# Kernel tuning notes

Measured on AMD Instinct MI355X. Metric: run time of the kernel, lower is better.

Reference implementation:

```python
import jax, jax.numpy as jnp
import numpy as np

H = 16  # heads
K_POLY = 3  # K from init


def setup_inputs() -> dict:
    key = jax.random.key(0)
    ks = jax.random.split(key, 6)
    B, N, D = 4, 1024, 1024
    s = 1.0 / np.sqrt(D)
    return {
        "x": jax.random.normal(ks[0], (B, N, D), jnp.float32),
        "Wq": jax.random.normal(ks[1], (D, D), jnp.float32) * s,
        "bq": jnp.zeros((D,), jnp.float32),
        "Wk": jax.random.normal(ks[2], (D, D), jnp.float32) * s,
        "bk": jnp.zeros((D,), jnp.float32),
        "Wv": jax.random.normal(ks[3], (D, D), jnp.float32) * s,
        "bv": jnp.zeros((D,), jnp.float32),
        "Wo": jax.random.normal(ks[4], (D, D), jnp.float32) * s,
        "bo": jnp.zeros((D,), jnp.float32),
        "w0": jnp.zeros((H,), jnp.float32),
        "w1": jnp.ones((H,), jnp.float32),
        "wK": jnp.zeros((H,), jnp.float32),
    }


def reference(x, Wq, bq, Wk, bk, Wv, bv, Wo, bo, w0, w1, wK):
    B, N, D = x.shape
    d = D // H
    # projections -> [B, H, N, d]
    def proj(W, b):
        return (x @ W + b).reshape(B, N, H, d).transpose(0, 2, 1, 3)
    q = proj(Wq, bq)
    k = proj(Wk, bk)
    v = proj(Wv, bv)
    att = jax.nn.softmax(jnp.einsum('bhnd,bhmd->bhnm', q, k) / jnp.sqrt(jnp.float32(d)), axis=-1)
    att2 = jnp.einsum('bhnm,bhmk->bhnk', att, att)  # att @ att
    attK = att + (K_POLY - 1) * (att2 - att)
    eye = jnp.eye(N, dtype=x.dtype)  # [N, N]
    gf = (w0[None, :, None, None] * eye[None, None]
          + w1[None, :, None, None] * att
          + wK[None, :, None, None] * attK)
    out = jnp.einsum('bhnm,bhmd->bhnd', gf, v)  # [B, H, N, d]
    out = out.transpose(0, 2, 1, 3).reshape(B, N, D)
    return out @ Wo + bo
```

## Files before the change

### kernel.cpp

```cpp
#include <hip/hip_runtime.h>

typedef unsigned short u16;
typedef unsigned int u32;
typedef __attribute__((ext_vector_type(8))) short short8;
typedef __attribute__((ext_vector_type(4))) float f32x4;

__device__ __forceinline__ u16 f2bf(float f) {
  union { float f; u32 u; } c; c.f = f;
  u32 u = c.u;
  u += 0x7fffu + ((u >> 16) & 1u);
  return (u16)(u >> 16);
}
__device__ __forceinline__ float bf2f(u16 h) {
  union { u32 u; float f; } c; c.u = ((u32)h) << 16;
  return c.f;
}

#define GLDS16(g, l)                                                          \
  __builtin_amdgcn_global_load_lds(                                           \
      (const __attribute__((address_space(1))) u32*)(g),                      \
      (__attribute__((address_space(3))) u32*)(l), 16, 0, 0)

#define EXP_SCALE 0.18033688011112042f

__global__ __launch_bounds__(256) void k_cast_x(const float* __restrict__ x,
                                                u16* __restrict__ xb) {
  int i = blockIdx.x * 256 + threadIdx.x;
  float4 v = ((const float4*)x)[i];
  short4 s;
  s.x = (short)f2bf(v.x); s.y = (short)f2bf(v.y);
  s.z = (short)f2bf(v.z); s.w = (short)f2bf(v.w);
  *(short4*)(xb + (size_t)i * 4) = s;
}

__global__ __launch_bounds__(256) void k_trans_w(
    const float* __restrict__ W0, const float* __restrict__ W1,
    const float* __restrict__ W2, const float* __restrict__ W3,
    u16* __restrict__ T0, u16* __restrict__ T1, u16* __restrict__ T2,
    u16* __restrict__ T3) {
  const float* W = blockIdx.z == 0 ? W0 : blockIdx.z == 1 ? W1 : blockIdx.z == 2 ? W2 : W3;
  u16* T = blockIdx.z == 0 ? T0 : blockIdx.z == 1 ? T1 : blockIdx.z == 2 ? T2 : T3;
  __shared__ float tile[32][33];
  int r0 = blockIdx.y * 32, c0 = blockIdx.x * 32;
  int tid = threadIdx.x;
  for (int i = tid; i < 1024; i += 256) {
    int r = i >> 5, c = i & 31;
    tile[r][c] = W[(size_t)(r0 + r) * 1024 + c0 + c];
  }
  __syncthreads();
  for (int i = tid; i < 1024; i += 256) {
    int r = i >> 5, c = i & 31;
    T[(size_t)(c0 + r) * 1024 + r0 + c] = f2bf(tile[c][r]);
  }
}

__device__ __forceinline__ void core128x128_p3(const u16* __restrict__ A,
                                               const u16* __restrict__ Bt, int K,
                                               f32x4 (&acc)[4][4], u16* As,
                                               u16* Bs) {
  const int tid = threadIdx.x;
  const int lane = tid & 63;
  const int wm = tid >> 7, wn = (tid >> 6) & 1;
  const int fr = lane & 15, fg = lane >> 4;
  const int sr = tid >> 2, sc = (tid & 3) * 8;
#pragma unroll
  for (int i = 0; i < 4; ++i)
#pragma unroll
    for (int j = 0; j < 4; ++j) acc[i][j] = f32x4{0.f, 0.f, 0.f, 0.f};

  auto stage = [&](int t, int slot) {
    u16* as = As + slot * 4096;
    u16* bs = Bs + slot * 4096;
    const int k0 = t * 32 + sc;
    GLDS16(A + (size_t)sr * K + k0, as + tid * 8);
    GLDS16(A + (size_t)(sr + 64) * K + k0, as + (256 + tid) * 8);
    GLDS16(Bt + (size_t)sr * K + k0, bs + tid * 8);
    GLDS16(Bt + (size_t)(sr + 64) * K + k0, bs + (256 + tid) * 8);
  };
  auto compute = [&](int slot) {
    const u16* as = As + slot * 4096;
    const u16* bs = Bs + slot * 4096;
    short8 af[4], bfv[4];
#pragma unroll
    for (int i = 0; i < 4; ++i)
      af[i] = *(const short8*)(as + (wm * 64 + i * 16 + fr) * 32 + fg * 8);
#pragma unroll
    for (int j = 0; j < 4; ++j)
      bfv[j] = *(const short8*)(bs + (wn * 64 + j * 16 + fr) * 32 + fg * 8);
#pragma unroll
    for (int i = 0; i < 4; ++i)
#pragma unroll
      for (int j = 0; j < 4; ++j)
        acc[i][j] = __builtin_amdgcn_mfma_f32_16x16x32_bf16(af[i], bfv[j],
                                                            acc[i][j], 0, 0, 0);
  };

  const int NS = K / 32;
  stage(0, 0);
  stage(1, 1);
  int cs = 0, ss = 2;
  for (int t = 0; t + 2 < NS; ++t) {
    asm volatile("s_waitcnt vmcnt(4) lgkmcnt(0)" ::: "memory");
    __builtin_amdgcn_s_barrier();
    asm volatile("" ::: "memory");
    stage(t + 2, ss);
    compute(cs);
    cs = cs == 2 ? 0 : cs + 1;
    ss = ss == 2 ? 0 : ss + 1;
  }
  asm volatile("s_waitcnt vmcnt(4) lgkmcnt(0)" ::: "memory");
  __builtin_amdgcn_s_barrier();
  asm volatile("" ::: "memory");
  compute(cs);
  cs = cs == 2 ? 0 : cs + 1;
  asm volatile("s_waitcnt vmcnt(0) lgkmcnt(0)" ::: "memory");
  __builtin_amdgcn_s_barrier();
  asm volatile("" ::: "memory");
  compute(cs);
}

__device__ __forceinline__ void core128x64_p3(const u16* __restrict__ A,
                                              const u16* __restrict__ Bt, int K,
                                              f32x4 (&acc)[2][4], u16* As,
                                              u16* Bs) {
  const int tid = threadIdx.x;
  const int lane = tid & 63;
  const int w = tid >> 6;
  const int fr = lane & 15, fg = lane >> 4;
  const int sr = tid >> 2, sc = (tid & 3) * 8;
#pragma unroll
  for (int i = 0; i < 2; ++i)
#pragma unroll
    for (int j = 0; j < 4; ++j) acc[i][j] = f32x4{0.f, 0.f, 0.f, 0.f};

  auto stage = [&](int t, int slot) {
    u16* as = As + slot * 4096;
    u16* bs = Bs + slot * 2048;
    const int k0 = t * 32 + sc;
    GLDS16(A + (size_t)sr * K + k0, as + tid * 8);
    GLDS16(A + (size_t)(sr + 64) * K + k0, as + (256 + tid) * 8);
    GLDS16(Bt + (size_t)sr * K + k0, bs + tid * 8);
  };
  auto compute = [&](int slot) {
    const u16* as = As + slot * 4096;
    const u16* bs = Bs + slot * 2048;
    short8 af[2], bfv[4];
#pragma unroll
    for (int i = 0; i < 2; ++i)
      af[i] = *(const short8*)(as + (w * 32 + i * 16 + fr) * 32 + fg * 8);
#pragma unroll
    for (int j = 0; j < 4; ++j)
      bfv[j] = *(const short8*)(bs + (j * 16 + fr) * 32 + fg * 8);
#pragma unroll
    for (int i = 0; i < 2; ++i)
#pragma unroll
      for (int j = 0; j < 4; ++j)
        acc[i][j] = __builtin_amdgcn_mfma_f32_16x16x32_bf16(af[i], bfv[j],
                                                            acc[i][j], 0, 0, 0);
  };

  const int NS = K / 32;
  stage(0, 0);
  stage(1, 1);
  int cs = 0, ss = 2;
  for (int t = 0; t + 2 < NS; ++t) {
    asm volatile("s_waitcnt vmcnt(3) lgkmcnt(0)" ::: "memory");
    __builtin_amdgcn_s_barrier();
    asm volatile("" ::: "memory");
    stage(t + 2, ss);
    compute(cs);
    cs = cs == 2 ? 0 : cs + 1;
    ss = ss == 2 ? 0 : ss + 1;
  }
  asm volatile("s_waitcnt vmcnt(3) lgkmcnt(0)" ::: "memory");
  __builtin_amdgcn_s_barrier();
  asm volatile("" ::: "memory");
  compute(cs);
  cs = cs == 2 ? 0 : cs + 1;
  asm volatile("s_waitcnt vmcnt(0) lgkmcnt(0)" ::: "memory");
  __builtin_amdgcn_s_barrier();
  asm volatile("" ::: "memory");
  compute(cs);
}

__global__ __launch_bounds__(256) void k_proj(
    const u16* __restrict__ xb, const u16* __restrict__ WqT,
    const u16* __restrict__ WkT, const u16* __restrict__ WvT,
    const float* __restrict__ bq, const float* __restrict__ bk,
    const float* __restrict__ bv, u16* __restrict__ qh, u16* __restrict__ kh,
    u16* __restrict__ vh, u16* __restrict__ vT) {
  __shared__ __align__(16) u16 As[3 * 128 * 32];
  __shared__ __align__(16) u16 Bs[3 * 128 * 32];
  const int li = blockIdx.x + 32 * (blockIdx.y + 8 * blockIdx.z);
  const int cx = li & 7, jb = li >> 3;
  const int m0 = (cx * 4 + (jb & 3)) * 128;
  const int n0 = ((jb >> 2) & 7) * 128;
  const int which = jb >> 5;
  const u16* Bt = which == 0 ? WqT : which == 1 ? WkT : WvT;
  const float* bias = which == 0 ? bq : which == 1 ? bk : bv;
  f32x4 acc[4][4];
  core128x128_p3(xb + (size_t)m0 * 1024, Bt + (size_t)n0 * 1024, 1024, acc, As, Bs);
  const int tid = threadIdx.x, lane = tid & 63;
  const int wm = tid >> 7, wn = (tid >> 6) & 1, fr = lane & 15, fg = lane >> 4;
#pragma unroll
  for (int i = 0; i < 4; ++i)
#pragma unroll
    for (int j2 = 0; j2 < 4; ++j2) {
      int n = n0 + wn * 64 + j2 * 16 + fr;
      float bb = bias[n];
      int h = n >> 6, dc = n & 63;
#pragma unroll
      for (int r = 0; r < 4; ++r) {
        int m = m0 + wm * 64 + i * 16 + fg * 4 + r;
        int b = m >> 10, nr = m & 1023;
        int z = b * 16 + h;
        float val = acc[i][j2][r] + bb;
        u16 bv16 = f2bf(val);
        if (which == 0) {
          qh[((size_t)z * 1024 + nr) * 64 + dc] = bv16;
        } else if (which == 1) {
          kh[((size_t)z * 1024 + nr) * 64 + dc] = bv16;
        } else {
          vh[((size_t)z * 1024 + nr) * 64 + dc] = bv16;
          vT[((size_t)z * 64 + dc) * 1024 + nr] = bv16;
        }
      }
    }
}

__global__ __launch_bounds__(256) void k_pass1(
    const u16* __restrict__ qh, const u16* __restrict__ kh,
    const u16* __restrict__ vT, u16* __restrict__ P1T,
    u16* __restrict__ P1h, float* __restrict__ mlinv) {
  __shared__ __align__(16) u16 Ks[64 * 64];
  __shared__ __align__(16) u16 Vs[64 * 64];
  __shared__ __align__(16) u16 Ps[4][16 * 64];
  const int li = blockIdx.x + 16 * blockIdx.y;
  const int cx = li & 7, jb = li >> 3;
  const int z = cx * 8 + (jb >> 4);
  const int m0 = (jb & 15) * 64;
  const int tid = threadIdx.x, lane = tid & 63, w = tid >> 6;
  const int fr = lane & 15, fg = lane >> 4;
  const int row0 = m0 + w * 16;
  const u16* qbase = qh + (size_t)z * 65536;
  const u16* kbase = kh + (size_t)z * 65536;
  const u16* vbase = vT + (size_t)z * 65536;
  u16* myP = &Ps[w][0];

  short8 qf[2];
#pragma unroll
  for (int kc = 0; kc < 2; ++kc)
    qf[kc] = *(const short8*)(qbase + (size_t)(row0 + fr) * 64 + (kc * 4 + fg) * 8);

  f32x4 o[4];
  float rs[4];
#pragma unroll
  for (int ct = 0; ct < 4; ++ct) o[ct] = f32x4{0.f, 0.f, 0.f, 0.f};
#pragma unroll
  for (int r = 0; r < 4; ++r) rs[r] = 0.f;

  for (int t = 0; t < 16; ++t) {
    const int kv0 = t * 64;
#pragma unroll
    for (int it = 0; it < 2; ++it) {
      int idx = it * 256 + tid;
      int row = idx >> 3, cc = idx & 7;
      GLDS16(kbase + (size_t)(kv0 + row) * 64 + ((cc ^ (row & 7)) * 8),
             Ks + idx * 8);
      GLDS16(vbase + (size_t)row * 1024 + kv0 + ((cc ^ (row & 7)) * 8),
             Vs + idx * 8);
    }
    __syncthreads();
#pragma unroll
    for (int ct = 0; ct < 4; ++ct) {
      int krow = ct * 16 + fr;
      short8 k0 = *(const short8*)(Ks + krow * 64 + ((fg ^ (krow & 7)) * 8));
      short8 k1 = *(const short8*)(Ks + krow * 64 + (((4 + fg) ^ (krow & 7)) * 8));
      f32x4 s = __builtin_amdgcn_mfma_f32_16x16x32_bf16(
          qf[0], k0, f32x4{0.f, 0.f, 0.f, 0.f}, 0, 0, 0);
      s = __builtin_amdgcn_mfma_f32_16x16x32_bf16(qf[1], k1, s, 0, 0, 0);
      int pcol = ct * 16 + fr;
      int cc = pcol >> 3;
#pragma unroll
      for (int r = 0; r < 4; ++r) {
        float e = __builtin_exp2f(s[r] * EXP_SCALE);
        rs[r] += e;
        int prow = fg * 4 + r;
        myP[prow * 64 + ((cc ^ (prow & 7)) * 8) + (pcol & 7)] = f2bf(e);
      }
    }
    asm volatile("s_waitcnt lgkmcnt(0)" ::: "memory");
    short8 p0 = *(const short8*)(myP + fr * 64 + ((fg ^ (fr & 7)) * 8));
    short8 p1 = *(const short8*)(myP + fr * 64 + (((4 + fg) ^ (fr & 7)) * 8));
#pragma unroll
    for (int ct = 0; ct < 4; ++ct) {
      int vrow = ct * 16 + fr;
      short8 v0 = *(const short8*)(Vs + vrow * 64 + ((fg ^ (vrow & 7)) * 8));
      short8 v1 = *(const short8*)(Vs + vrow * 64 + (((4 + fg) ^ (vrow & 7)) * 8));
      o[ct] = __builtin_amdgcn_mfma_f32_16x16x32_bf16(p0, v0, o[ct], 0, 0, 0);
      o[ct] = __builtin_amdgcn_mfma_f32_16x16x32_bf16(p1, v1, o[ct], 0, 0, 0);
    }
    __syncthreads();
  }
#pragma unroll
  for (int off = 1; off < 16; off <<= 1)
#pragma unroll
    for (int r = 0; r < 4; ++r) rs[r] += __shfl_xor(rs[r], off, 64);
  float linv[4];
#pragma unroll
  for (int r = 0; r < 4; ++r) linv[r] = 1.f / rs[r];
#pragma unroll
  for (int ct = 0; ct < 4; ++ct) {
    union { u16 u[4]; short4 s4; } pk;
#pragma unroll
    for (int r = 0; r < 4; ++r) {
      u16 b_ = f2bf(o[ct][r] * linv[r]);
      pk.u[r] = b_;
      myP[(fg * 4 + r) * 64 + ct * 16 + fr] = b_;
    }
    *(short4*)(P1T + ((size_t)z * 64 + ct * 16 + fr) * 1024 + row0 + fg * 4) =
        pk.s4;
  }
  asm volatile("s_waitcnt lgkmcnt(0)" ::: "memory");
  {
    int r_ = lane >> 2;
#pragma unroll
    for (int ch2 = 0; ch2 < 2; ++ch2) {
      int ch = (lane & 3) * 2 + ch2;
      int4 vv = *(const int4*)(myP + r_ * 64 + ch * 8);
      *(int4*)(P1h + ((size_t)z * 1024 + row0 + r_) * 64 + ch * 8) = vv;
    }
  }
  if (fr == 0) {
#pragma unroll
    for (int r = 0; r < 4; ++r)
      mlinv[(size_t)z * 1024 + row0 + fg * 4 + r] = linv[r];
  }
}

__global__ __launch_bounds__(256) void k_pass2(
    const u16* __restrict__ qh, const u16* __restrict__ kh,
    const u16* __restrict__ P1T, const u16* __restrict__ vh,
    const u16* __restrict__ P1h, const float* __restrict__ mlinv,
    const float* __restrict__ w0, const float* __restrict__ w1,
    const float* __restrict__ wK, u16* __restrict__ OH) {
  __shared__ __align__(16) u16 Ks[64 * 64];
  __shared__ __align__(16) u16 Ts[64 * 64];
  __shared__ __align__(16) u16 Ps[4][16 * 64];
  const int li = blockIdx.x + 16 * blockIdx.y;
  const int cx = li & 7, jb = li >> 3;
  const int z = cx * 8 + (jb >> 4);
  const int m0 = (jb & 15) * 64;
  const int tid = threadIdx.x, lane = tid & 63, w = tid >> 6;
  const int fr = lane & 15, fg = lane >> 4;
  const int row0 = m0 + w * 16;
  const int h = z & 15, b = z >> 4;
  const float cw0 = w0[h], cw1 = w1[h] - wK[h], cw2 = 2.f * wK[h];
  const u16* qbase = qh + (size_t)z * 65536;
  const u16* kbase = kh + (size_t)z * 65536;
  const u16* tbase = P1T + (size_t)z * 65536;
  u16* myP = &Ps[w][0];

  short8 qf[2];
#pragma unroll
  for (int kc = 0; kc < 2; ++kc)
    qf[kc] = *(const short8*)(qbase + (size_t)(row0 + fr) * 64 + (kc * 4 + fg) * 8);
  float lrow[4];
#pragma unroll
  for (int r = 0; r < 4; ++r)
    lrow[r] = mlinv[(size_t)z * 1024 + row0 + fg * 4 + r];
  f32x4 o[4];
#pragma unroll
  for (int ct = 0; ct < 4; ++ct) o[ct] = f32x4{0.f, 0.f, 0.f, 0.f};

  for (int t = 0; t < 16; ++t) {
    const int kv0 = t * 64;
#pragma unroll
    for (int it = 0; it < 2; ++it) {
      int idx = it * 256 + tid;
      int row = idx >> 3, cc = idx & 7;
      GLDS16(kbase + (size_t)(kv0 + row) * 64 + ((cc ^ (row & 7)) * 8),
             Ks + idx * 8);
      GLDS16(tbase + (size_t)row * 1024 + kv0 + ((cc ^ (row & 7)) * 8),
             Ts + idx * 8);
    }
    __syncthreads();
#pragma unroll
    for (int ct = 0; ct < 4; ++ct) {
      int krow = ct * 16 + fr;
      short8 k0 = *(const short8*)(Ks + krow * 64 + ((fg ^ (krow & 7)) * 8));
      short8 k1 = *(const short8*)(Ks + krow * 64 + (((4 + fg) ^ (krow & 7)) * 8));
      f32x4 s = __builtin_amdgcn_mfma_f32_16x16x32_bf16(
          qf[0], k0, f32x4{0.f, 0.f, 0.f, 0.f}, 0, 0, 0);
      s = __builtin_amdgcn_mfma_f32_16x16x32_bf16(qf[1], k1, s, 0, 0, 0);
      int pcol = ct * 16 + fr;
      int cc = pcol >> 3;
#pragma unroll
      for (int r = 0; r < 4; ++r) {
        float p = __builtin_exp2f(s[r] * EXP_SCALE) * lrow[r];
        int prow = fg * 4 + r;
        myP[prow * 64 + ((cc ^ (prow & 7)) * 8) + (pcol & 7)] = f2bf(p);
      }
    }
    asm volatile("s_waitcnt lgkmcnt(0)" ::: "memory");
    short8 p0 = *(const short8*)(myP + fr * 64 + ((fg ^ (fr & 7)) * 8));
    short8 p1 = *(const short8*)(myP + fr * 64 + (((4 + fg) ^ (fr & 7)) * 8));
#pragma unroll
    for (int ct = 0; ct < 4; ++ct) {
      int vrow = ct * 16 + fr;
      short8 v0 = *(const short8*)(Ts + vrow * 64 + ((fg ^ (vrow & 7)) * 8));
      short8 v1 = *(const short8*)(Ts + vrow * 64 + (((4 + fg) ^ (vrow & 7)) * 8));
      o[ct] = __builtin_amdgcn_mfma_f32_16x16x32_bf16(p0, v0, o[ct], 0, 0, 0);
      o[ct] = __builtin_amdgcn_mfma_f32_16x16x32_bf16(p1, v1, o[ct], 0, 0, 0);
    }
    __syncthreads();
  }
#pragma unroll
  for (int ct = 0; ct < 4; ++ct)
#pragma unroll
    for (int r = 0; r < 4; ++r)
      myP[(fg * 4 + r) * 64 + ct * 16 + fr] = f2bf(o[ct][r]);
  asm volatile("s_waitcnt lgkmcnt(0)" ::: "memory");
  {
    int r_ = lane >> 2;
    const u16* vp = vh + ((size_t)z * 1024 + row0 + r_) * 64;
    const u16* pp = P1h + ((size_t)z * 1024 + row0 + r_) * 64;
    u16* op = OH + ((size_t)b * 1024 + row0 + r_) * 1024 + h * 64;
#pragma unroll
    for (int ch2 = 0; ch2 < 2; ++ch2) {
      int ch = (lane & 3) * 2 + ch2;
      short8 pv = *(const short8*)(myP + r_ * 64 + ch * 8);
      short8 vv = *(const short8*)(vp + ch * 8);
      short8 p1 = *(const short8*)(pp + ch * 8);
      short8 res;
#pragma unroll
      for (int e = 0; e < 8; ++e) {
        float f = cw0 * bf2f((u16)vv[e]) + cw1 * bf2f((u16)p1[e]) +
                  cw2 * bf2f((u16)pv[e]);
        res[e] = (short)f2bf(f);
      }
      *(short8*)(op + ch * 8) = res;
    }
  }
}

__global__ __launch_bounds__(256) void k_final(const u16* __restrict__ OH,
                                               const u16* __restrict__ WoT,
                                               const float* __restrict__ bo,
                                               float* __restrict__ out) {
  __shared__ __align__(16) u16 As[3 * 128 * 32];
  __shared__ __align__(16) u16 Bs[3 * 64 * 32];
  const int li = blockIdx.x + 32 * blockIdx.y;
  const int cx = li & 7, jb = li >> 3;
  const int m0 = (cx * 4 + (jb & 3)) * 128;
  const int n0 = (jb >> 2) * 64;
  f32x4 acc[2][4];
  core128x64_p3(OH + (size_t)m0 * 1024, WoT + (size_t)n0 * 1024, 1024, acc, As, Bs);
  const int tid = threadIdx.x, lane = tid & 63, w = tid >> 6;
  const int fr = lane & 15, fg = lane >> 4;
#pragma unroll
  for (int i = 0; i < 2; ++i)
#pragma unroll
    for (int j2 = 0; j2 < 4; ++j2) {
      int n = n0 + j2 * 16 + fr;
      float bb = bo[n];
#pragma unroll
      for (int r = 0; r < 4; ++r) {
        int m = m0 + w * 32 + i * 16 + fg * 4 + r;
        out[(size_t)m * 1024 + n] = acc[i][j2][r] + bb;
      }
    }
}

extern "C" void kernel_launch(void* const* d_in, const int* in_sizes, int n_in,
                              void* d_out, int out_size, void* d_ws,
                              size_t ws_size, hipStream_t stream) {
  const float* x = (const float*)d_in[0];
  const float* Wq = (const float*)d_in[1];
  const float* bq = (const float*)d_in[2];
  const float* Wk = (const float*)d_in[3];
  const float* bk = (const float*)d_in[4];
  const float* Wv = (const float*)d_in[5];
  const float* bv = (const float*)d_in[6];
  const float* Wo = (const float*)d_in[7];
  const float* bo = (const float*)d_in[8];
  const float* w0 = (const float*)d_in[9];
  const float* w1 = (const float*)d_in[10];
  const float* wK = (const float*)d_in[11];
  float* out = (float*)d_out;

  char* ws = (char*)d_ws;
  const size_t MB = 1ull << 20;
  u16* xb  = (u16*)(ws);
  u16* WqT = (u16*)(ws + 8 * MB);
  u16* WkT = (u16*)(ws + 10 * MB);
  u16* WvT = (u16*)(ws + 12 * MB);
  u16* WoT = (u16*)(ws + 14 * MB);
  u16* qh  = (u16*)(ws + 16 * MB);
  u16* kh  = (u16*)(ws + 24 * MB);
  u16* vh  = (u16*)(ws + 32 * MB);
  u16* vT  = (u16*)(ws + 40 * MB);
  u16* P1T = (u16*)(ws + 48 * MB);
  u16* P1h = (u16*)(ws + 56 * MB);
  u16* OH  = (u16*)(ws + 64 * MB);
  float* mlinv = (float*)(ws + 72 * MB);

  hipLaunchKernelGGL(k_cast_x, dim3(4096), dim3(256), 0, stream, x, xb);
  hipLaunchKernelGGL(k_trans_w, dim3(32, 32, 4), dim3(256), 0, stream, Wq, Wk,
                     Wv, Wo, WqT, WkT, WvT, WoT);
  hipLaunchKernelGGL(k_proj, dim3(32, 8, 3), dim3(256), 0, stream, xb, WqT, WkT,
                     WvT, bq, bk, bv, qh, kh, vh, vT);
  hipLaunchKernelGGL(k_pass1, dim3(16, 64), dim3(256), 0, stream, qh, kh, vT,
                     P1T, P1h, mlinv);
  hipLaunchKernelGGL(k_pass2, dim3(16, 64), dim3(256), 0, stream, qh, kh, P1T,
                     vh, P1h, mlinv, w0, w1, wK, OH);
  hipLaunchKernelGGL(k_final, dim3(32, 16), dim3(256), 0, stream, OH, WoT, bo,
                     out);
}
```

Measured before the change: 156.2 us.

## Rewrite QKV projection GEMM with 256x256 tiles and swizzled LDS

The QKV projection kernel now uses 512-thread blocks that each compute a 256x256 output tile with a 64-wide K step. Loads go through double-buffered, XOR-swizzled LDS to avoid bank conflicts, replacing the earlier 128x128 tile with a 3-stage pipeline and 32-wide K step. Larger tiles raise data reuse per global load. The trade-off is only 192 blocks, fewer than the CU count, a large LDS footprint per block, and a full vmcnt(0) wait every iteration.

```diff
diff --git a/kernel.cpp b/kernel.cpp
--- a/kernel.cpp
+++ b/kernel.cpp
@@ -54,69 +54,109 @@
   }
 }
 
-__device__ __forceinline__ void core128x128_p3(const u16* __restrict__ A,
-                                               const u16* __restrict__ Bt, int K,
-                                               f32x4 (&acc)[4][4], u16* As,
-                                               u16* Bs) {
-  const int tid = threadIdx.x;
-  const int lane = tid & 63;
-  const int wm = tid >> 7, wn = (tid >> 6) & 1;
-  const int fr = lane & 15, fg = lane >> 4;
-  const int sr = tid >> 2, sc = (tid & 3) * 8;
-#pragma unroll
-  for (int i = 0; i < 4; ++i)
+__global__ __launch_bounds__(512, 2) void k_proj(
+    const u16* __restrict__ xb, const u16* __restrict__ WqT,
+    const u16* __restrict__ WkT, const u16* __restrict__ WvT,
+    const float* __restrict__ bq, const float* __restrict__ bk,
+    const float* __restrict__ bv, u16* __restrict__ qh, u16* __restrict__ kh,
+    u16* __restrict__ vh, u16* __restrict__ vT) {
+  __shared__ __align__(16) u16 As[2][256 * 64];
+  __shared__ __align__(16) u16 Bs[2][256 * 64];
+  const int m0 = blockIdx.x * 256, n0 = blockIdx.y * 256;
+  const int which = blockIdx.z;
+  const u16* Ag = xb + (size_t)m0 * 1024;
+  const u16* Bg = (which == 0 ? WqT : which == 1 ? WkT : WvT) + (size_t)n0 * 1024;
+  const float* bias = which == 0 ? bq : which == 1 ? bk : bv;
+  const int tid = threadIdx.x, lane = tid & 63, wid = tid >> 6;
+  const int wm = wid >> 2, wn = wid & 3, fr = lane & 15, fg = lane >> 4;
+
+  f32x4 acc[8][4];
+#pragma unroll
+  for (int i = 0; i < 8; ++i)
 #pragma unroll
     for (int j = 0; j < 4; ++j) acc[i][j] = f32x4{0.f, 0.f, 0.f, 0.f};
 
-  auto stage = [&](int t, int slot) {
-    u16* as = As + slot * 4096;
-    u16* bs = Bs + slot * 4096;
-    const int k0 = t * 32 + sc;
-    GLDS16(A + (size_t)sr * K + k0, as + tid * 8);
-    GLDS16(A + (size_t)(sr + 64) * K + k0, as + (256 + tid) * 8);
-    GLDS16(Bt + (size_t)sr * K + k0, bs + tid * 8);
-    GLDS16(Bt + (size_t)(sr + 64) * K + k0, bs + (256 + tid) * 8);
+  auto stage = [&](int kt, int buf) {
+#pragma unroll
+    for (int L = 0; L < 4; ++L) {
+      int q = L * 512 + tid;
+      int row = q >> 3, c = q & 7;
+      int kc = c ^ (row & 7);
+      GLDS16(Ag + (size_t)row * 1024 + kt * 64 + kc * 8, &As[buf][q * 8]);
+    }
+#pragma unroll
+    for (int L = 0; L < 4; ++L) {
+      int q = L * 512 + tid;
+      int row = q >> 3, c = q & 7;
+      int kc = c ^ (row & 7);
+      GLDS16(Bg + (size_t)row * 1024 + kt * 64 + kc * 8, &Bs[buf][q * 8]);
+    }
   };
-  auto compute = [&](int slot) {
-    const u16* as = As + slot * 4096;
-    const u16* bs = Bs + slot * 4096;
-    short8 af[4], bfv[4];
-#pragma unroll
-    for (int i = 0; i < 4; ++i)
-      af[i] = *(const short8*)(as + (wm * 64 + i * 16 + fr) * 32 + fg * 8);
-#pragma unroll
-    for (int j = 0; j < 4; ++j)
-      bfv[j] = *(const short8*)(bs + (wn * 64 + j * 16 + fr) * 32 + fg * 8);
-#pragma unroll
-    for (int i = 0; i < 4; ++i)
-#pragma unroll
-      for (int j = 0; j < 4; ++j)
-        acc[i][j] = __builtin_amdgcn_mfma_f32_16x16x32_bf16(af[i], bfv[j],
-                                                            acc[i][j], 0, 0, 0);
-  };
-
-  const int NS = K / 32;
+
   stage(0, 0);
-  stage(1, 1);
-  int cs = 0, ss = 2;
-  for (int t = 0; t + 2 < NS; ++t) {
-    asm volatile("s_waitcnt vmcnt(4) lgkmcnt(0)" ::: "memory");
+  asm volatile("s_waitcnt vmcnt(0)" ::: "memory");
+  __builtin_amdgcn_s_barrier();
+  asm volatile("" ::: "memory");
+  int cur = 0;
+  for (int kt = 0; kt < 16; ++kt) {
+    if (kt + 1 < 16) stage(kt + 1, cur ^ 1);
+    const u16* as = &As[cur][0];
+    const u16* bs = &Bs[cur][0];
+#pragma unroll
+    for (int ks = 0; ks < 2; ++ks) {
+      short8 bf_[4];
+#pragma unroll
+      for (int j = 0; j < 4; ++j) {
+        int row = wn * 64 + j * 16 + fr;
+        int kk = ks * 4 + fg;
+        bf_[j] = *(const short8*)(bs + row * 64 + ((kk ^ (row & 7)) * 8));
+      }
+#pragma unroll
+      for (int mh = 0; mh < 2; ++mh) {
+        short8 af_[4];
+#pragma unroll
+        for (int i = 0; i < 4; ++i) {
+          int row = wm * 128 + mh * 64 + i * 16 + fr;
+          int kk = ks * 4 + fg;
+          af_[i] = *(const short8*)(as + row * 64 + ((kk ^ (row & 7)) * 8));
+        }
+#pragma unroll
+        for (int i = 0; i < 4; ++i)
+#pragma unroll
+          for (int j = 0; j < 4; ++j)
+            acc[mh * 4 + i][j] = __builtin_amdgcn_mfma_f32_16x16x32_bf16(
+                af_[i], bf_[j], acc[mh * 4 + i][j], 0, 0, 0);
+      }
+    }
+    asm volatile("s_waitcnt vmcnt(0) lgkmcnt(0)" ::: "memory");
     __builtin_amdgcn_s_barrier();
     asm volatile("" ::: "memory");
-    stage(t + 2, ss);
-    compute(cs);
-    cs = cs == 2 ? 0 : cs + 1;
-    ss = ss == 2 ? 0 : ss + 1;
-  }
-  asm volatile("s_waitcnt vmcnt(4) lgkmcnt(0)" ::: "memory");
-  __builtin_amdgcn_s_barrier();
-  asm volatile("" ::: "memory");
-  compute(cs);
-  cs = cs == 2 ? 0 : cs + 1;
-  asm volatile("s_waitcnt vmcnt(0) lgkmcnt(0)" ::: "memory");
-  __builtin_amdgcn_s_barrier();
-  asm volatile("" ::: "memory");
-  compute(cs);
+    cur ^= 1;
+  }
+#pragma unroll
+  for (int f = 0; f < 8; ++f)
+#pragma unroll
+    for (int j2 = 0; j2 < 4; ++j2) {
+      int n = n0 + wn * 64 + j2 * 16 + fr;
+      float bb = bias[n];
+      int h = n >> 6, dc = n & 63;
+#pragma unroll
+      for (int r = 0; r < 4; ++r) {
+        int m = m0 + wm * 128 + (f >> 2) * 64 + (f & 3) * 16 + fg * 4 + r;
+        int b = m >> 10, nr = m & 1023;
+        int z = b * 16 + h;
+        float val = acc[f][j2][r] + bb;
+        u16 bv16 = f2bf(val);
+        if (which == 0) {
+          qh[((size_t)z * 1024 + nr) * 64 + dc] = bv16;
+        } else if (which == 1) {
+          kh[((size_t)z * 1024 + nr) * 64 + dc] = bv16;
+        } else {
+          vh[((size_t)z * 1024 + nr) * 64 + dc] = bv16;
+          vT[((size_t)z * 64 + dc) * 1024 + nr] = bv16;
+        }
+      }
+    }
 }
 
 __device__ __forceinline__ void core128x64_p3(const u16* __restrict__ A,
@@ -181,51 +221,6 @@
   __builtin_amdgcn_s_barrier();
   asm volatile("" ::: "memory");
   compute(cs);
-}
-
-__global__ __launch_bounds__(256) void k_proj(
-    const u16* __restrict__ xb, const u16* __restrict__ WqT,
-    const u16* __restrict__ WkT, const u16* __restrict__ WvT,
-    const float* __restrict__ bq, const float* __restrict__ bk,
-    const float* __restrict__ bv, u16* __restrict__ qh, u16* __restrict__ kh,
-    u16* __restrict__ vh, u16* __restrict__ vT) {
-  __shared__ __align__(16) u16 As[3 * 128 * 32];
-  __shared__ __align__(16) u16 Bs[3 * 128 * 32];
-  const int li = blockIdx.x + 32 * (blockIdx.y + 8 * blockIdx.z);
-  const int cx = li & 7, jb = li >> 3;
-  const int m0 = (cx * 4 + (jb & 3)) * 128;
-  const int n0 = ((jb >> 2) & 7) * 128;
-  const int which = jb >> 5;
-  const u16* Bt = which == 0 ? WqT : which == 1 ? WkT : WvT;
-  const float* bias = which == 0 ? bq : which == 1 ? bk : bv;
-  f32x4 acc[4][4];
-  core128x128_p3(xb + (size_t)m0 * 1024, Bt + (size_t)n0 * 1024, 1024, acc, As, Bs);
-  const int tid = threadIdx.x, lane = tid & 63;
-  const int wm = tid >> 7, wn = (tid >> 6) & 1, fr = lane & 15, fg = lane >> 4;
-#pragma unroll
-  for (int i = 0; i < 4; ++i)
-#pragma unroll
-    for (int j2 = 0; j2 < 4; ++j2) {
-      int n = n0 + wn * 64 + j2 * 16 + fr;
-      float bb = bias[n];
-      int h = n >> 6, dc = n & 63;
-#pragma unroll
-      for (int r = 0; r < 4; ++r) {
-        int m = m0 + wm * 64 + i * 16 + fg * 4 + r;
-        int b = m >> 10, nr = m & 1023;
-        int z = b * 16 + h;
-        float val = acc[i][j2][r] + bb;
-        u16 bv16 = f2bf(val);
-        if (which == 0) {
-          qh[((size_t)z * 1024 + nr) * 64 + dc] = bv16;
-        } else if (which == 1) {
-          kh[((size_t)z * 1024 + nr) * 64 + dc] = bv16;
-        } else {
-          vh[((size_t)z * 1024 + nr) * 64 + dc] = bv16;
-          vT[((size_t)z * 64 + dc) * 1024 + nr] = bv16;
-        }
-      }
-    }
 }
 
 __global__ __launch_bounds__(256) void k_pass1(
@@ -508,7 +503,7 @@
   hipLaunchKernelGGL(k_cast_x, dim3(4096), dim3(256), 0, stream, x, xb);
   hipLaunchKernelGGL(k_trans_w, dim3(32, 32, 4), dim3(256), 0, stream, Wq, Wk,
                      Wv, Wo, WqT, WkT, WvT, WoT);
-  hipLaunchKernelGGL(k_proj, dim3(32, 8, 3), dim3(256), 0, stream, xb, WqT, WkT,
+  hipLaunchKernelGGL(k_proj, dim3(16, 4, 3), dim3(512), 0, stream, xb, WqT, WkT,
                      WvT, bq, bk, bv, qh, kh, vh, vT);
   hipLaunchKernelGGL(k_pass1, dim3(16, 64), dim3(256), 0, stream, qh, kh, vT,
                      P1T, P1h, mlinv);
```

After: 177.6 us. 13.7% more time.
